# Optimization experiments

Hardware: AMD Instinct MI355X
Metric: run time of the kernel (lower is better)

The kernel has to match this reference:

```python
import jax, jax.numpy as jnp
import numpy as np

N, E, G, T = 4096, 16384, 128, 100
DIMS = [(5, 64), (64, 128), (128, 256)]
EPS = 1e-5


def setup_inputs() -> dict:
    key = jax.random.key(0)
    ks = iter(jax.random.split(key, 64))
    d = {}
    d["x"] = jax.random.normal(next(ks), (N, 5), jnp.float32)
    d["edge_index"] = jax.random.randint(next(ks), (2, E), 0, N, jnp.int64)
    d["edge_attr"] = jax.random.uniform(next(ks), (E, 3), jnp.float32)
    d["batch_seg"] = jnp.sort(jax.random.randint(next(ks), (N,), 0, G, jnp.int64))
    for l, (cin, cout) in enumerate(DIMS, start=1):
        d[f"l{l}_W1"] = jax.random.normal(next(ks), (3, 32), jnp.float32) * 0.3
        d[f"l{l}_b1"] = jnp.zeros((32,), jnp.float32)
        d[f"l{l}_W2"] = jax.random.normal(next(ks), (32, cin * cout), jnp.float32) * 0.05
        d[f"l{l}_b2"] = jnp.zeros((cin * cout,), jnp.float32)
        d[f"l{l}_root"] = jax.random.normal(next(ks), (cin, cout), jnp.float32) * 0.1
        d[f"l{l}_bias"] = jnp.zeros((cout,), jnp.float32)
        d[f"bn{l}_g"] = jnp.ones((cout,), jnp.float32)
        d[f"bn{l}_b"] = jnp.zeros((cout,), jnp.float32)
        d[f"bn{l}_m"] = jax.random.normal(next(ks), (cout,), jnp.float32) * 0.01
        d[f"bn{l}_v"] = jax.random.uniform(next(ks), (cout,), jnp.float32, 0.5, 1.5)
    d["mlp_W"] = jax.random.normal(next(ks), (256, T), jnp.float32) * 0.06
    d["mlp_b"] = jnp.zeros((T,), jnp.float32)
    return d


def _nnconv(h, src, dst, edge_attr, W1, b1, W2, b2, root, bias, cin, cout):
    # edge MLP -> per-edge weight matrix [E, cin, cout]
    ew = (jax.nn.relu(edge_attr @ W1 + b1) @ W2 + b2).reshape(-1, cin, cout)
    msg = jnp.einsum('ei,eio->eo', h[src], ew)  # gather + per-edge matmul
    ssum = jax.ops.segment_sum(msg, dst, num_segments=N)
    cnt = jax.ops.segment_sum(jnp.ones((msg.shape[0],), msg.dtype), dst, num_segments=N)
    agg = ssum / jnp.maximum(cnt, 1.0)[:, None]  # scatter-mean
    return h @ root + agg + bias


def _bn(h, g, b, m, v):
    return g * (h - m) * jax.lax.rsqrt(v + EPS) + b


def reference(x, edge_index, edge_attr, batch_seg,
              l1_W1, l1_b1, l1_W2, l1_b2, l1_root, l1_bias, bn1_g, bn1_b, bn1_m, bn1_v,
              l2_W1, l2_b1, l2_W2, l2_b2, l2_root, l2_bias, bn2_g, bn2_b, bn2_m, bn2_v,
              l3_W1, l3_b1, l3_W2, l3_b2, l3_root, l3_bias, bn3_g, bn3_b, bn3_m, bn3_v,
              mlp_W, mlp_b):
    src, dst = edge_index[0], edge_index[1]
    h = _nnconv(x, src, dst, edge_attr, l1_W1, l1_b1, l1_W2, l1_b2, l1_root, l1_bias, 5, 64)
    h = jax.nn.relu(_bn(h, bn1_g, bn1_b, bn1_m, bn1_v))
    h = _nnconv(h, src, dst, edge_attr, l2_W1, l2_b1, l2_W2, l2_b2, l2_root, l2_bias, 64, 128)
    h = jax.nn.relu(_bn(h, bn2_g, bn2_b, bn2_m, bn2_v))
    h = _nnconv(h, src, dst, edge_attr, l3_W1, l3_b1, l3_W2, l3_b2, l3_root, l3_bias, 128, 256)
    h = jax.nn.relu(_bn(h, bn3_g, bn3_b, bn3_m, bn3_v))
    # global mean pool over graphs
    psum = jax.ops.segment_sum(h, batch_seg, num_segments=G)
    pcnt = jax.ops.segment_sum(jnp.ones((N,), h.dtype), batch_seg, num_segments=G)
    pooled = psum / jnp.maximum(pcnt, 1.0)[:, None]
    out = pooled @ mlp_W + mlp_b
    return jnp.where(out > 0, out, 0.1 * out)  # LeakyReLU(0.1)
```

## Files before the change

### kernel.cpp

```cpp
#include <hip/hip_runtime.h>
#include <cstdint>
#include <cstddef>

#define BN_EPS 1e-5f

typedef short bf16x8 __attribute__((ext_vector_type(8)));
typedef float f32x4  __attribute__((ext_vector_type(4)));
typedef unsigned short u16x8 __attribute__((ext_vector_type(8)));

__device__ __forceinline__ uint16_t f2bf_rte(float f) {
  uint32_t u = __float_as_uint(f);
  uint32_t r = u + 0x7fffu + ((u >> 16) & 1u);
  return (uint16_t)(r >> 16);
}
__device__ __forceinline__ float bf2f(uint16_t h) {
  return __uint_as_float(((uint32_t)h) << 16);
}
__device__ __forceinline__ void split_bf(float v, uint16_t& hi, uint16_t& lo) {
  hi = f2bf_rte(v);
  lo = f2bf_rte(v - bf2f(hi));
}

__device__ __forceinline__ void glds16(const uint16_t* g, uint16_t* l) {
  __builtin_amdgcn_global_load_lds(
      (const __attribute__((address_space(1))) uint32_t*)(const void*)g,
      (__attribute__((address_space(3))) uint32_t*)(void*)l, 16, 0, 0);
}

__global__ void zero_i32_k(int* p, int n) {
  int i = blockIdx.x * blockDim.x + threadIdx.x;
  if (i < n) p[i] = 0;
}

__global__ void hist_k(const int* __restrict__ dst, int* __restrict__ cnt, int E) {
  int e = blockIdx.x * blockDim.x + threadIdx.x;
  if (e < E) atomicAdd(&cnt[dst[e]], 1);
}

__global__ __launch_bounds__(1024) void scan_k(const int* __restrict__ cnt,
                                               int* __restrict__ offsets,
                                               int* __restrict__ cursor,
                                               int N, int total) {
  __shared__ int part[1024];
  int t = threadIdx.x;
  int a0 = cnt[4*t+0], a1 = cnt[4*t+1], a2 = cnt[4*t+2], a3 = cnt[4*t+3];
  part[t] = a0 + a1 + a2 + a3;
  __syncthreads();
  for (int off = 1; off < 1024; off <<= 1) {
    int v = (t >= off) ? part[t - off] : 0;
    __syncthreads();
    part[t] += v;
    __syncthreads();
  }
  int excl = (t == 0) ? 0 : part[t-1];
  int o0 = excl, o1 = o0 + a0, o2 = o1 + a1, o3 = o2 + a2;
  offsets[4*t+0] = o0; offsets[4*t+1] = o1; offsets[4*t+2] = o2; offsets[4*t+3] = o3;
  cursor [4*t+0] = o0; cursor [4*t+1] = o1; cursor [4*t+2] = o2; cursor [4*t+3] = o3;
  if (t == 0) offsets[N] = total;
}

__global__ void scatter_k(const int* __restrict__ dst, int* __restrict__ cursor,
                          int* __restrict__ csr, int E) {
  int e = blockIdx.x * blockDim.x + threadIdx.x;
  if (e < E) {
    int d = dst[e];
    int pos = atomicAdd(&cursor[d], 1);
    csr[pos] = e;
  }
}

__global__ void build_W2pT_k(const float* __restrict__ W2, const float* __restrict__ b2,
                             const float* __restrict__ root,
                             uint16_t* __restrict__ Bhi, uint16_t* __restrict__ Blo,
                             int cin, int cout, int Kpad) {
  int idx = blockIdx.x * blockDim.x + threadIdx.x;
  int total = cout * Kpad;
  if (idx >= total) return;
  int o  = idx / Kpad;
  int ki = idx - o * Kpad;
  float v = 0.f;
  if (ki < 34 * cin) {
    int k = ki / cin;
    int i = ki - k * cin;
    if (k < 32)       v = W2[(size_t)k * cin * cout + (size_t)i * cout + o];
    else if (k == 32) v = b2[(size_t)i * cout + o];
    else              v = root[(size_t)i * cout + o];
  }
  uint16_t hi, lo;
  split_bf(v, hi, lo);
  Bhi[idx] = hi;
  Blo[idx] = lo;
}

template<int CIN>
__global__ __launch_bounds__(256) void build_S_vec_k(const float* __restrict__ h,
                                                     const float* __restrict__ ea,
                                                     const float* __restrict__ W1,
                                                     const float* __restrict__ b1,
                                                     const int* __restrict__ src,
                                                     const int* __restrict__ csr,
                                                     const int* __restrict__ offsets,
                                                     uint16_t* __restrict__ Shi,
                                                     uint16_t* __restrict__ Slo,
                                                     int Kpad) {
  constexpr int CH = 8;
  constexpr int K1 = 33 * CIN;
  constexpr int NCH = K1 / 8;
  constexpr int NP = (NCH + 255) / 256;
  __shared__ float hs[CH][CIN];
  __shared__ float zs[CH][33];
  __shared__ int   es[CH];
  const int n = blockIdx.x;
  const int tid = threadIdx.x;
  const int base = offsets[n];
  const int deg  = offsets[n+1] - base;
  const float scale = 1.f / fmaxf((float)deg, 1.f);
  float acc[NP][8];
#pragma unroll
  for (int p = 0; p < NP; p++)
#pragma unroll
    for (int j = 0; j < 8; j++) acc[p][j] = 0.f;

  for (int c0 = 0; c0 < deg; c0 += CH) {
    const int cc = min(CH, deg - c0);
    if (tid < cc) es[tid] = csr[base + c0 + tid];
    __syncthreads();
    for (int idx = tid; idx < cc * CIN; idx += 256) {
      int slot = idx / CIN, i = idx - slot * CIN;
      hs[slot][i] = h[(size_t)src[es[slot]] * CIN + i];
    }
    for (int idx = tid; idx < cc * 33; idx += 256) {
      int slot = idx / 33, k = idx - slot * 33;
      float v;
      if (k == 32) v = 1.f;
      else {
        int e = es[slot];
        v = fmaxf(ea[e*3+0] * W1[k] + ea[e*3+1] * W1[32 + k] + ea[e*3+2] * W1[64 + k] + b1[k], 0.f);
      }
      zs[slot][k] = v;
    }
    __syncthreads();
#pragma unroll
    for (int p = 0; p < NP; p++) {
      int ch = p * 256 + tid;
      if (ch < NCH) {
        int ki0 = ch * 8;
        int k  = ki0 / CIN;
        int i0 = ki0 & (CIN - 1);
        for (int c = 0; c < cc; c++) {
          float zv = zs[c][k];
          float4 h0 = *(const float4*)&hs[c][i0];
          float4 h1 = *(const float4*)&hs[c][i0 + 4];
          acc[p][0] += zv * h0.x; acc[p][1] += zv * h0.y;
          acc[p][2] += zv * h0.z; acc[p][3] += zv * h0.w;
          acc[p][4] += zv * h1.x; acc[p][5] += zv * h1.y;
          acc[p][6] += zv * h1.z; acc[p][7] += zv * h1.w;
        }
      }
    }
    __syncthreads();
  }
  const size_t rowb = (size_t)n * Kpad;
#pragma unroll
  for (int p = 0; p < NP; p++) {
    int ch = p * 256 + tid;
    if (ch < NCH) {
      u16x8 hv, lv;
#pragma unroll
      for (int j = 0; j < 8; j++) {
        uint16_t hi, lo;
        split_bf(acc[p][j] * scale, hi, lo);
        hv[j] = hi; lv[j] = lo;
      }
      *(u16x8*)(Shi + rowb + ch * 8) = hv;
      *(u16x8*)(Slo + rowb + ch * 8) = lv;
    }
  }
  for (int c = tid; c < CIN / 8; c += 256) {
    int i0 = c * 8;
    float4 a = *(const float4*)&h[(size_t)n * CIN + i0];
    float4 b = *(const float4*)&h[(size_t)n * CIN + i0 + 4];
    float vals[8] = {a.x, a.y, a.z, a.w, b.x, b.y, b.z, b.w};
    u16x8 hv, lv;
#pragma unroll
    for (int j = 0; j < 8; j++) {
      uint16_t hi, lo;
      split_bf(vals[j], hi, lo);
      hv[j] = hi; lv[j] = lo;
    }
    *(u16x8*)(Shi + rowb + K1 + i0) = hv;
    *(u16x8*)(Slo + rowb + K1 + i0) = lv;
  }
  for (int ki = 34 * CIN + tid; ki < Kpad; ki += 256) {
    Shi[rowb + ki] = 0;
    Slo[rowb + ki] = 0;
  }
}

__global__ __launch_bounds__(256) void build_S5_k(const float* __restrict__ h,
                                                  const float* __restrict__ ea,
                                                  const float* __restrict__ W1,
                                                  const float* __restrict__ b1,
                                                  const int* __restrict__ src,
                                                  const int* __restrict__ csr,
                                                  const int* __restrict__ offsets,
                                                  uint16_t* __restrict__ Shi,
                                                  uint16_t* __restrict__ Slo,
                                                  int Kpad) {
  constexpr int CIN = 5, CH = 8;
  constexpr int K1 = 33 * CIN;
  constexpr int KT = 34 * CIN;
  __shared__ float hs[CH][CIN];
  __shared__ float zs[CH][33];
  __shared__ int   es[CH];
  const int n = blockIdx.x;
  const int tid = threadIdx.x;
  const int base = offsets[n];
  const int deg  = offsets[n+1] - base;
  const float scale = 1.f / fmaxf((float)deg, 1.f);
  float acc = 0.f;

  for (int c0 = 0; c0 < deg; c0 += CH) {
    const int cc = min(CH, deg - c0);
    if (tid < cc) es[tid] = csr[base + c0 + tid];
    __syncthreads();
    for (int idx = tid; idx < cc * CIN; idx += 256) {
      int slot = idx / CIN, i = idx - slot * CIN;
      hs[slot][i] = h[(size_t)src[es[slot]] * CIN + i];
    }
    for (int idx = tid; idx < cc * 33; idx += 256) {
      int slot = idx / 33, k = idx - slot * 33;
      float v;
      if (k == 32) v = 1.f;
      else {
        int e = es[slot];
        v = fmaxf(ea[e*3+0] * W1[k] + ea[e*3+1] * W1[32 + k] + ea[e*3+2] * W1[64 + k] + b1[k], 0.f);
      }
      zs[slot][k] = v;
    }
    __syncthreads();
    if (tid < K1) {
      int k = tid / CIN, i = tid - (tid / CIN) * CIN;
      float a = acc;
      for (int c = 0; c < cc; c++) a += zs[c][k] * hs[c][i];
      acc = a;
    }
    __syncthreads();
  }
  const size_t rowb = (size_t)n * Kpad;
  if (tid < K1) {
    uint16_t hi, lo;
    split_bf(acc * scale, hi, lo);
    Shi[rowb + tid] = hi;
    Slo[rowb + tid] = lo;
  }
  if (tid < CIN) {
    uint16_t hi, lo;
    split_bf(h[(size_t)n * CIN + tid], hi, lo);
    Shi[rowb + K1 + tid] = hi;
    Slo[rowb + K1 + tid] = lo;
  }
  for (int ki = KT + tid; ki < Kpad; ki += 256) {
    Shi[rowb + ki] = 0;
    Slo[rowb + ki] = 0;
  }
}

template<int BN, int KS>
__global__ __launch_bounds__(256, 1) void mfma_gemm2_k(const uint16_t* __restrict__ Ahi,
                                                       const uint16_t* __restrict__ Alo,
                                                       const uint16_t* __restrict__ Bhi,
                                                       const uint16_t* __restrict__ Blo,
                                                       float* __restrict__ Cpart,
                                                       int Kpad, int Ncol, int M,
                                                       int totalIters) {
  constexpr int BM = 128;
  constexpr int FN = BN / 32;
  constexpr int SLOTS = KS / 8;
  constexpr int RPC = 2048 / KS;
  constexpr int NCA = BM / RPC;
  constexpr int NCB = BN / RPC;
  constexpr int OAH = 0;
  constexpr int OAL = BM * KS;
  constexpr int OBH = 2 * BM * KS;
  constexpr int OBL = 2 * BM * KS + BN * KS;
  constexpr int BUFSZ = (2 * BM + 2 * BN) * KS;
  __shared__ uint16_t smem[2 * BUFSZ] __attribute__((aligned(16)));

  const int m0 = blockIdx.x * BM;
  const int n0 = blockIdx.y * BN;
  const int SK = gridDim.z;
  const int z  = blockIdx.z;
  const int itBeg = (int)((long long)totalIters * z / SK);
  const int itEnd = (int)((long long)totalIters * (z + 1) / SK);
  const int nsteps = itEnd - itBeg;

  const int tid  = threadIdx.x;
  const int lane = tid & 63;
  const int wave = tid >> 6;
  const int wm = wave & 1, wn = wave >> 1;
  const int q  = lane >> 4;
  const int mr = lane & 15;

  const int srow  = tid / SLOTS;
  const int sslot = tid & (SLOTS - 1);
  const int sx    = (KS == 64) ? (srow & 7) : ((srow >> 1) & 3);
  const int swz   = (sslot ^ sx) * 8;
  size_t aoff[NCA], boff[NCB];
#pragma unroll
  for (int c = 0; c < NCA; c++)
    aoff[c] = (size_t)(m0 + c * RPC + srow) * Kpad + swz + (size_t)itBeg * KS;
#pragma unroll
  for (int c = 0; c < NCB; c++)
    boff[c] = (size_t)(n0 + c * RPC + srow) * Kpad + swz + (size_t)itBeg * KS;
  const int wlds = wave << 9;

  f32x4 acc[4][FN];
#pragma unroll
  for (int a = 0; a < 4; a++)
#pragma unroll
    for (int b = 0; b < FN; b++) acc[a][b] = (f32x4)0.f;

  auto stage = [&](int buf, int t) {
    uint16_t* base = smem + buf * BUFSZ;
    const size_t ka = (size_t)t * KS;
#pragma unroll
    for (int c = 0; c < NCA; c++) {
      glds16(Ahi + aoff[c] + ka, base + OAH + c * 2048 + wlds);
      glds16(Alo + aoff[c] + ka, base + OAL + c * 2048 + wlds);
    }
#pragma unroll
    for (int c = 0; c < NCB; c++) {
      glds16(Bhi + boff[c] + ka, base + OBH + c * 2048 + wlds);
      glds16(Blo + boff[c] + ka, base + OBL + c * 2048 + wlds);
    }
  };

  const int xr = (KS == 64) ? (mr & 7) : ((mr >> 1) & 3);

  if (nsteps > 0) stage(0, 0);
  for (int t = 0; t < nsteps; t++) {
    __syncthreads();
    if (t + 1 < nsteps) stage((t & 1) ^ 1, t + 1);
    const uint16_t* B_ = smem + (t & 1) * BUFSZ;
#pragma unroll
    for (int ks = 0; ks < KS / 32; ks++) {
      const int e0 = (ks * 32 + q * 8) ^ (xr << 3);
      bf16x8 ah[4], al[4], bh[FN], bl[FN];
#pragma unroll
      for (int f = 0; f < 4; f++) {
        const int row = wm * 64 + f * 16 + mr;
        ah[f] = *(const bf16x8*)&B_[OAH + row * KS + e0];
        al[f] = *(const bf16x8*)&B_[OAL + row * KS + e0];
      }
#pragma unroll
      for (int f = 0; f < FN; f++) {
        const int row = wn * (BN / 2) + f * 16 + mr;
        bh[f] = *(const bf16x8*)&B_[OBH + row * KS + e0];
        bl[f] = *(const bf16x8*)&B_[OBL + row * KS + e0];
      }
#pragma unroll
      for (int fm = 0; fm < 4; fm++)
#pragma unroll
        for (int fn = 0; fn < FN; fn++) {
          acc[fm][fn] = __builtin_amdgcn_mfma_f32_16x16x32_bf16(ah[fm], bh[fn], acc[fm][fn], 0, 0, 0);
          acc[fm][fn] = __builtin_amdgcn_mfma_f32_16x16x32_bf16(ah[fm], bl[fn], acc[fm][fn], 0, 0, 0);
          acc[fm][fn] = __builtin_amdgcn_mfma_f32_16x16x32_bf16(al[fm], bh[fn], acc[fm][fn], 0, 0, 0);
        }
    }
  }

  float* Cz = Cpart + (size_t)z * M * Ncol;
#pragma unroll
  for (int fm = 0; fm < 4; fm++) {
#pragma unroll
    for (int reg = 0; reg < 4; reg++) {
      const int row = m0 + wm * 64 + fm * 16 + q * 4 + reg;
#pragma unroll
      for (int fn = 0; fn < FN; fn++) {
        const int col = n0 + wn * (BN / 2) + fn * 16 + mr;
        Cz[(size_t)row * Ncol + col] = acc[fm][fn][reg];
      }
    }
  }
}

__global__ void epilogue_k(const float* __restrict__ Cpart, int SK, size_t plane4,
                           int Ncol,
                           const float* __restrict__ bias, const float* __restrict__ bg,
                           const float* __restrict__ bb, const float* __restrict__ bnm,
                           const float* __restrict__ bnv,
                           float* __restrict__ C, int total4) {
  int i = blockIdx.x * blockDim.x + threadIdx.x;
  if (i >= total4) return;
  float4 v = {0.f, 0.f, 0.f, 0.f};
  for (int z = 0; z < SK; z++) {
    float4 p = *((const float4*)Cpart + (size_t)z * plane4 + i);
    v.x += p.x; v.y += p.y; v.z += p.z; v.w += p.w;
  }
  int col0 = (i * 4) % Ncol;
  float o[4] = {v.x, v.y, v.z, v.w};
#pragma unroll
  for (int j = 0; j < 4; j++) {
    int c = col0 + j;
    float s = bg[c] * rsqrtf(bnv[c] + BN_EPS);
    float val = (o[j] + bias[c] - bnm[c]) * s + bb[c];
    o[j] = fmaxf(val, 0.f);
  }
  float4 r = {o[0], o[1], o[2], o[3]};
  *((float4*)C + i) = r;
}

__global__ __launch_bounds__(256) void pool_final_k(const float* __restrict__ h,
                                                    const int* __restrict__ seg,
                                                    const float* __restrict__ W,
                                                    const float* __restrict__ b,
                                                    float* __restrict__ out,
                                                    int N, int T) {
  __shared__ float pooled[256];
  const int g = blockIdx.x, tid = threadIdx.x;
  int lo = 0, hi = N;
  while (lo < hi) { int mid = (lo + hi) >> 1; if (seg[mid] < g) lo = mid + 1; else hi = mid; }
  int lo2 = lo, hi2 = N;
  while (lo2 < hi2) { int mid = (lo2 + hi2) >> 1; if (seg[mid] < g + 1) lo2 = mid + 1; else hi2 = mid; }
  const int cnt = lo2 - lo;
  const float inv = 1.f / fmaxf((float)cnt, 1.f);
  float s = 0.f;
  for (int n = lo; n < lo2; n++) s += h[(size_t)n * 256 + tid];
  pooled[tid] = s * inv;
  __syncthreads();
  if (tid < T) {
    float acc = b[tid];
    for (int o = 0; o < 256; o++) acc += pooled[o] * W[(size_t)o * T + tid];
    out[(size_t)g * T + tid] = (acc > 0.f) ? acc : 0.1f * acc;
  }
}

extern "C" void kernel_launch(void* const* d_in, const int* in_sizes, int n_in,
                              void* d_out, int out_size, void* d_ws, size_t ws_size,
                              hipStream_t stream) {
  const float* x   = (const float*)d_in[0];
  const int*   ei  = (const int*)d_in[1];
  const float* ea  = (const float*)d_in[2];
  const int*   seg = (const int*)d_in[3];

  const int N = in_sizes[0] / 5;
  const int E = in_sizes[2] / 3;
  const int T = in_sizes[35];
  const int G = out_size / T;
  const int* src = ei;
  const int* dst = ei + E;

  const float *W1[3], *b1[3], *W2[3], *b2[3], *root[3], *bias[3];
  const float *bng[3], *bnb[3], *bnm[3], *bnv[3];
  for (int l = 0; l < 3; l++) {
    int base = 4 + l * 10;
    W1[l]   = (const float*)d_in[base + 0];
    b1[l]   = (const float*)d_in[base + 1];
    W2[l]   = (const float*)d_in[base + 2];
    b2[l]   = (const float*)d_in[base + 3];
    root[l] = (const float*)d_in[base + 4];
    bias[l] = (const float*)d_in[base + 5];
    bng[l]  = (const float*)d_in[base + 6];
    bnb[l]  = (const float*)d_in[base + 7];
    bnm[l]  = (const float*)d_in[base + 8];
    bnv[l]  = (const float*)d_in[base + 9];
  }
  const float* mlpW = (const float*)d_in[34];
  const float* mlpb = (const float*)d_in[35];

  char* p = (char*)d_ws;
  auto carve = [&](size_t bytes) -> char* {
    char* r = p;
    p += (bytes + 255) & ~(size_t)255;
    return r;
  };
  const int KPADMAX = 4352;
  int*      cnt     = (int*)carve((size_t)N * 4);
  int*      offsets = (int*)carve((size_t)(N + 1) * 4);
  int*      cursor  = (int*)carve((size_t)N * 4);
  int*      csr     = (int*)carve((size_t)E * 4);
  uint16_t* Whi     = (uint16_t*)carve((size_t)256 * KPADMAX * 2);
  uint16_t* Wlo     = (uint16_t*)carve((size_t)256 * KPADMAX * 2);
  uint16_t* Shi     = (uint16_t*)carve((size_t)N * KPADMAX * 2);
  uint16_t* Slo     = (uint16_t*)carve((size_t)N * KPADMAX * 2);
  float*    Cpart   = (float*)carve((size_t)8 * N * 256 * 4);
  float*    hA      = (float*)carve((size_t)N * 256 * 4);
  float*    hB      = (float*)carve((size_t)N * 128 * 4);

  zero_i32_k<<<(N + 255) / 256, 256, 0, stream>>>(cnt, N);
  hist_k<<<(E + 255) / 256, 256, 0, stream>>>(dst, cnt, E);
  scan_k<<<1, 1024, 0, stream>>>(cnt, offsets, cursor, N, E);
  scatter_k<<<(E + 255) / 256, 256, 0, stream>>>(dst, cursor, csr, E);

  const int cins[3]   = {5, 64, 128};
  const int couts[3]  = {64, 128, 256};
  const int kpads[3]  = {192, 2176, 4352};
  const int sks[3]    = {3, 8, 8};
  const int ksteps[3] = {64, 64, 32};

  const float* hin = x;
  float* houts[3] = {hA, hB, hA};

  for (int l = 0; l < 3; l++) {
    int cin = cins[l], cout = couts[l], Kpad = kpads[l], SK = sks[l];
    int iters = Kpad / ksteps[l];
    build_W2pT_k<<<(cout * Kpad + 255) / 256, 256, 0, stream>>>(W2[l], b2[l], root[l],
                                                                Whi, Wlo, cin, cout, Kpad);
    if (cin == 5)
      build_S5_k<<<N, 256, 0, stream>>>(hin, ea, W1[l], b1[l], src, csr, offsets, Shi, Slo, Kpad);
    else if (cin == 64)
      build_S_vec_k<64><<<N, 256, 0, stream>>>(hin, ea, W1[l], b1[l], src, csr, offsets, Shi, Slo, Kpad);
    else
      build_S_vec_k<128><<<N, 256, 0, stream>>>(hin, ea, W1[l], b1[l], src, csr, offsets, Shi, Slo, Kpad);

    if (cout == 256) {
      dim3 grid(N / 128, 1, SK);
      mfma_gemm2_k<256, 32><<<grid, 256, 0, stream>>>(Shi, Slo, Whi, Wlo, Cpart,
                                                      Kpad, cout, N, iters);
    } else if (cout == 128) {
      dim3 grid(N / 128, 1, SK);
      mfma_gemm2_k<128, 64><<<grid, 256, 0, stream>>>(Shi, Slo, Whi, Wlo, Cpart,
                                                      Kpad, cout, N, iters);
    } else {
      dim3 grid(N / 128, 1, SK);
      mfma_gemm2_k<64, 64><<<grid, 256, 0, stream>>>(Shi, Slo, Whi, Wlo, Cpart,
                                                     Kpad, cout, N, iters);
    }

    int total4 = N * cout / 4;
    epilogue_k<<<(total4 + 255) / 256, 256, 0, stream>>>(Cpart, SK, (size_t)N * cout / 4, cout,
                                                         bias[l], bng[l], bnb[l], bnm[l], bnv[l],
                                                         houts[l], total4);
    hin = houts[l];
  }

  pool_final_k<<<G, 256, 0, stream>>>(hA, seg, mlpW, mlpb, (float*)d_out, N, T);
}
```

Measured before the change: 282.5 us.

## Fuse CSR build into one kernel, batch weight packing, retile layer-3 GEMM

Replaces the zero/histogram/scan/scatter kernel chain with a single 1024-thread block that builds the CSR using shared-memory atomics. The three per-layer weight-packing launches become one kernel writing into separate per-layer buffers. The cout=256 GEMM now uses the 128x64 tile with a grid split over output columns and split-K cut from 8 to 4. The aim is fewer launches and better GEMM tiling, at the cost of serialising the CSR build on one block.

```diff
diff --git a/kernel.cpp b/kernel.cpp
--- a/kernel.cpp
+++ b/kernel.cpp
@@ -27,23 +27,18 @@
       (__attribute__((address_space(3))) uint32_t*)(void*)l, 16, 0, 0);
 }
 
-__global__ void zero_i32_k(int* p, int n) {
-  int i = blockIdx.x * blockDim.x + threadIdx.x;
-  if (i < n) p[i] = 0;
-}
-
-__global__ void hist_k(const int* __restrict__ dst, int* __restrict__ cnt, int E) {
-  int e = blockIdx.x * blockDim.x + threadIdx.x;
-  if (e < E) atomicAdd(&cnt[dst[e]], 1);
-}
-
-__global__ __launch_bounds__(1024) void scan_k(const int* __restrict__ cnt,
-                                               int* __restrict__ offsets,
-                                               int* __restrict__ cursor,
-                                               int N, int total) {
+__global__ __launch_bounds__(1024) void csr_all_k(const int* __restrict__ dst,
+                                                  int* __restrict__ offsets,
+                                                  int* __restrict__ csr,
+                                                  int N, int E) {
+  __shared__ int cntS[4096];
   __shared__ int part[1024];
-  int t = threadIdx.x;
-  int a0 = cnt[4*t+0], a1 = cnt[4*t+1], a2 = cnt[4*t+2], a3 = cnt[4*t+3];
+  const int t = threadIdx.x;
+  for (int i = t; i < N; i += 1024) cntS[i] = 0;
+  __syncthreads();
+  for (int e = t; e < E; e += 1024) atomicAdd(&cntS[dst[e]], 1);
+  __syncthreads();
+  int a0 = cntS[4*t+0], a1 = cntS[4*t+1], a2 = cntS[4*t+2], a3 = cntS[4*t+3];
   part[t] = a0 + a1 + a2 + a3;
   __syncthreads();
   for (int off = 1; off < 1024; off <<= 1) {
@@ -54,30 +49,23 @@
   }
   int excl = (t == 0) ? 0 : part[t-1];
   int o0 = excl, o1 = o0 + a0, o2 = o1 + a1, o3 = o2 + a2;
+  cntS[4*t+0] = o0; cntS[4*t+1] = o1; cntS[4*t+2] = o2; cntS[4*t+3] = o3;
   offsets[4*t+0] = o0; offsets[4*t+1] = o1; offsets[4*t+2] = o2; offsets[4*t+3] = o3;
-  cursor [4*t+0] = o0; cursor [4*t+1] = o1; cursor [4*t+2] = o2; cursor [4*t+3] = o3;
-  if (t == 0) offsets[N] = total;
-}
-
-__global__ void scatter_k(const int* __restrict__ dst, int* __restrict__ cursor,
-                          int* __restrict__ csr, int E) {
-  int e = blockIdx.x * blockDim.x + threadIdx.x;
-  if (e < E) {
+  if (t == 0) offsets[N] = E;
+  __syncthreads();
+  for (int e = t; e < E; e += 1024) {
     int d = dst[e];
-    int pos = atomicAdd(&cursor[d], 1);
+    int pos = atomicAdd(&cntS[d], 1);
     csr[pos] = e;
   }
 }
 
-__global__ void build_W2pT_k(const float* __restrict__ W2, const float* __restrict__ b2,
-                             const float* __restrict__ root,
-                             uint16_t* __restrict__ Bhi, uint16_t* __restrict__ Blo,
-                             int cin, int cout, int Kpad) {
-  int idx = blockIdx.x * blockDim.x + threadIdx.x;
-  int total = cout * Kpad;
-  if (idx >= total) return;
-  int o  = idx / Kpad;
-  int ki = idx - o * Kpad;
+__device__ __forceinline__ void w_elem(const float* __restrict__ W2, const float* __restrict__ b2,
+                                       const float* __restrict__ root,
+                                       uint16_t* __restrict__ Hi, uint16_t* __restrict__ Lo,
+                                       int cin, int cout, int Kpad, int li) {
+  int o  = li / Kpad;
+  int ki = li - o * Kpad;
   float v = 0.f;
   if (ki < 34 * cin) {
     int k = ki / cin;
@@ -88,8 +76,24 @@
   }
   uint16_t hi, lo;
   split_bf(v, hi, lo);
-  Bhi[idx] = hi;
-  Blo[idx] = lo;
+  Hi[li] = hi;
+  Lo[li] = lo;
+}
+
+__global__ void build_W3_k(const float* __restrict__ W2a, const float* __restrict__ b2a,
+                           const float* __restrict__ roota, uint16_t* __restrict__ Hia,
+                           uint16_t* __restrict__ Loa,
+                           const float* __restrict__ W2b, const float* __restrict__ b2b,
+                           const float* __restrict__ rootb, uint16_t* __restrict__ Hib,
+                           uint16_t* __restrict__ Lob,
+                           const float* __restrict__ W2c, const float* __restrict__ b2c,
+                           const float* __restrict__ rootc, uint16_t* __restrict__ Hic,
+                           uint16_t* __restrict__ Loc,
+                           int e0, int e1, int e2) {
+  int idx = blockIdx.x * blockDim.x + threadIdx.x;
+  if (idx < e0)      w_elem(W2a, b2a, roota, Hia, Loa, 5,   64,  192,  idx);
+  else if (idx < e1) w_elem(W2b, b2b, rootb, Hib, Lob, 64,  128, 2176, idx - e0);
+  else if (idx < e2) w_elem(W2c, b2c, rootc, Hic, Loc, 128, 256, 4352, idx - e1);
 }
 
 template<int CIN>
@@ -476,37 +480,44 @@
     return r;
   };
   const int KPADMAX = 4352;
-  int*      cnt     = (int*)carve((size_t)N * 4);
+  const int cins[3]   = {5, 64, 128};
+  const int couts[3]  = {64, 128, 256};
+  const int kpads[3]  = {192, 2176, 4352};
+  const int sks[3]    = {3, 8, 4};
+
   int*      offsets = (int*)carve((size_t)(N + 1) * 4);
-  int*      cursor  = (int*)carve((size_t)N * 4);
   int*      csr     = (int*)carve((size_t)E * 4);
-  uint16_t* Whi     = (uint16_t*)carve((size_t)256 * KPADMAX * 2);
-  uint16_t* Wlo     = (uint16_t*)carve((size_t)256 * KPADMAX * 2);
+  uint16_t* WhiL[3]; uint16_t* WloL[3];
+  for (int l = 0; l < 3; l++) {
+    WhiL[l] = (uint16_t*)carve((size_t)couts[l] * kpads[l] * 2);
+    WloL[l] = (uint16_t*)carve((size_t)couts[l] * kpads[l] * 2);
+  }
   uint16_t* Shi     = (uint16_t*)carve((size_t)N * KPADMAX * 2);
   uint16_t* Slo     = (uint16_t*)carve((size_t)N * KPADMAX * 2);
   float*    Cpart   = (float*)carve((size_t)8 * N * 256 * 4);
   float*    hA      = (float*)carve((size_t)N * 256 * 4);
   float*    hB      = (float*)carve((size_t)N * 128 * 4);
 
-  zero_i32_k<<<(N + 255) / 256, 256, 0, stream>>>(cnt, N);
-  hist_k<<<(E + 255) / 256, 256, 0, stream>>>(dst, cnt, E);
-  scan_k<<<1, 1024, 0, stream>>>(cnt, offsets, cursor, N, E);
-  scatter_k<<<(E + 255) / 256, 256, 0, stream>>>(dst, cursor, csr, E);
-
-  const int cins[3]   = {5, 64, 128};
-  const int couts[3]  = {64, 128, 256};
-  const int kpads[3]  = {192, 2176, 4352};
-  const int sks[3]    = {3, 8, 8};
-  const int ksteps[3] = {64, 64, 32};
+  csr_all_k<<<1, 1024, 0, stream>>>(dst, offsets, csr, N, E);
+
+  {
+    int t0 = couts[0] * kpads[0];
+    int t1 = couts[1] * kpads[1];
+    int t2 = couts[2] * kpads[2];
+    int e0 = t0, e1 = t0 + t1, e2 = t0 + t1 + t2;
+    build_W3_k<<<(e2 + 255) / 256, 256, 0, stream>>>(
+        W2[0], b2[0], root[0], WhiL[0], WloL[0],
+        W2[1], b2[1], root[1], WhiL[1], WloL[1],
+        W2[2], b2[2], root[2], WhiL[2], WloL[2],
+        e0, e1, e2);
+  }
 
   const float* hin = x;
   float* houts[3] = {hA, hB, hA};
 
   for (int l = 0; l < 3; l++) {
     int cin = cins[l], cout = couts[l], Kpad = kpads[l], SK = sks[l];
-    int iters = Kpad / ksteps[l];
-    build_W2pT_k<<<(cout * Kpad + 255) / 256, 256, 0, stream>>>(W2[l], b2[l], root[l],
-                                                                Whi, Wlo, cin, cout, Kpad);
+    int iters = Kpad / 64;
     if (cin == 5)
       build_S5_k<<<N, 256, 0, stream>>>(hin, ea, W1[l], b1[l], src, csr, offsets, Shi, Slo, Kpad);
     else if (cin == 64)
@@ -514,17 +525,13 @@
     else
       build_S_vec_k<128><<<N, 256, 0, stream>>>(hin, ea, W1[l], b1[l], src, csr, offsets, Shi, Slo, Kpad);
 
-    if (cout == 256) {
-      dim3 grid(N / 128, 1, SK);
-      mfma_gemm2_k<256, 32><<<grid, 256, 0, stream>>>(Shi, Slo, Whi, Wlo, Cpart,
-                                                      Kpad, cout, N, iters);
-    } else if (cout == 128) {
-      dim3 grid(N / 128, 1, SK);
-      mfma_gemm2_k<128, 64><<<grid, 256, 0, stream>>>(Shi, Slo, Whi, Wlo, Cpart,
+    if (cout >= 128) {
+      dim3 grid(N / 128, cout / 128, SK);
+      mfma_gemm2_k<128, 64><<<grid, 256, 0, stream>>>(Shi, Slo, WhiL[l], WloL[l], Cpart,
                                                       Kpad, cout, N, iters);
     } else {
       dim3 grid(N / 128, 1, SK);
-      mfma_gemm2_k<64, 64><<<grid, 256, 0, stream>>>(Shi, Slo, Whi, Wlo, Cpart,
+      mfma_gemm2_k<64, 64><<<grid, 256, 0, stream>>>(Shi, Slo, WhiL[l], WloL[l], Cpart,
                                                      Kpad, cout, N, iters);
     }
 
```

Result: no change. 281.1 us (-0.5%).
